# Kernel optimization log

Measured on AMD Instinct MI355X. Metric: run time of the kernel, lower is better.

## Reference

```python
import jax, jax.numpy as jnp
import numpy as np
from functools import partial

N_NODES = 50000
N_EDGES = 1_600_000
T = 9
F_IN = 128
HID = 128
OUT = 1


def setup_inputs() -> dict:
    key = jax.random.key(0)
    ks = jax.random.split(key, 8)
    s = 0.05
    return {
        "x_seq": jax.random.normal(ks[0], (T, N_NODES, F_IN), dtype=jnp.float32),
        "edge_index": jax.random.randint(ks[1], (2, N_EDGES), 0, N_NODES, dtype=jnp.int64),
        "W_gcn": jax.random.normal(ks[2], (F_IN, HID), dtype=jnp.float32) * s,
        "b_gcn": jnp.zeros((HID,), dtype=jnp.float32),
        "W_ih": jax.random.normal(ks[3], (4 * HID, HID), dtype=jnp.float32) * s,
        "W_hh": jax.random.normal(ks[4], (4 * HID, HID), dtype=jnp.float32) * s,
        "b_ih": jnp.zeros((4 * HID,), dtype=jnp.float32),
        "b_hh": jnp.zeros((4 * HID,), dtype=jnp.float32),
        "W_fc": jax.random.normal(ks[5], (HID, OUT), dtype=jnp.float32) * s,
        "b_fc": jnp.zeros((OUT,), dtype=jnp.float32),
    }


def reference(x_seq, edge_index, W_gcn, b_gcn, W_ih, W_hh, b_ih, b_hh, W_fc, b_fc):
    T_, N, _ = x_seq.shape
    H = W_hh.shape[1]

    # --- GCNConv normalization (add self-loops, symmetric deg^-1/2) ---
    loops = jnp.arange(N, dtype=edge_index.dtype)
    src = jnp.concatenate([edge_index[0], loops])  # [E+N]
    dst = jnp.concatenate([edge_index[1], loops])  # [E+N]
    deg = jax.ops.segment_sum(jnp.ones_like(dst, dtype=x_seq.dtype), dst, num_segments=N)
    dinv = jnp.where(deg > 0, jax.lax.rsqrt(deg), 0.0)
    norm = dinv[src] * dinv[dst]  # [E+N]

    # Linear transform for all timesteps at once (dense GEMM)
    xw = jnp.einsum("tnf,fh->tnh", x_seq, W_gcn)  # [T, N, H]

    # Per-timestep gather -> scale -> scatter-add (scan to bound memory)
    def gcn_step(_, xw_t):
        msg = xw_t[src] * norm[:, None]                       # [E+N, H]
        agg = jax.ops.segment_sum(msg, dst, num_segments=N)   # [N, H]
        return None, jax.nn.relu(agg + b_gcn)                 # dropout: eval mode (identity)

    _, emb = jax.lax.scan(gcn_step, None, xw)  # [T, N, H]

    # --- single-layer LSTM over time, nodes as batch (PyTorch gate order i,f,g,o) ---
    def lstm_step(carry, x_t):
        h_prev, c_prev = carry
        gates = x_t @ W_ih.T + h_prev @ W_hh.T + (b_ih + b_hh)  # [N, 4H]
        i, f, g, o = jnp.split(gates, 4, axis=-1)
        i, f, o = jax.nn.sigmoid(i), jax.nn.sigmoid(f), jax.nn.sigmoid(o)
        g = jnp.tanh(g)
        c = f * c_prev + i * g
        h = o * jnp.tanh(c)
        return (h, c), h

    init = (jnp.zeros((N, H), x_seq.dtype), jnp.zeros((N, H), x_seq.dtype))
    _, hs = jax.lax.scan(lstm_step, init, emb)  # [T, N, H]

    lstm_out = jnp.transpose(hs, (1, 0, 2))  # [N, T, H] (batch_first)
    # final_dropout: eval mode (identity)
    return lstm_out @ W_fc + b_fc  # [N, T, OUT]
```

## Files before the change

kernel.cpp:

```cpp
#include <hip/hip_runtime.h>
#include <math.h>

#define NN 50000
#define TT 9
#define FD 128
#define HD 128

using short8 = __attribute__((ext_vector_type(8))) short;
using half8  = __attribute__((ext_vector_type(8))) _Float16;
using f32x4  = __attribute__((ext_vector_type(4))) float;
using f32x2  = __attribute__((ext_vector_type(2))) float;
using half2v = __attribute__((ext_vector_type(2))) _Float16;
typedef unsigned short ushort_t;

__device__ inline float fast_sigmoid(float x) {
  x = fminf(fmaxf(x, -30.f), 30.f);
  return 1.f / (1.f + __expf(-x));
}
__device__ inline float fast_tanh(float x) {
  x = fminf(fmaxf(x, -15.f), 15.f);
  float e = __expf(2.f * x);
  return (e - 1.f) / (e + 1.f);
}

__global__ void k_detect(const unsigned int* __restrict__ e32, int nchk,
                         int* __restrict__ stride_out) {
  __shared__ unsigned int red[256];
  unsigned int acc = 0;
  for (int i = threadIdx.x; i < nchk; i += 256) acc |= e32[2 * i + 1];
  red[threadIdx.x] = acc;
  __syncthreads();
  for (int s = 128; s > 0; s >>= 1) {
    if ((int)threadIdx.x < s) red[threadIdx.x] |= red[threadIdx.x + s];
    __syncthreads();
  }
  if (threadIdx.x == 0) stride_out[0] = (red[0] == 0u) ? 2 : 1;
}

__global__ void k_count(const unsigned int* __restrict__ e32, int E,
                        const int* __restrict__ stridep, int* __restrict__ cnt) {
  int e = blockIdx.x * 256 + threadIdx.x;
  if (e >= E) return;
  int st = stridep[0];
  int d = (int)e32[(size_t)(E + e) * st];
  atomicAdd(&cnt[d], 1);
}

__global__ void k_dinv(const int* __restrict__ cnt, float* __restrict__ dinv, int N) {
  int n = blockIdx.x * 256 + threadIdx.x;
  if (n < N) dinv[n] = rsqrtf((float)(cnt[n] + 1));
}

__global__ void k_scan(const int* __restrict__ cnt, int* __restrict__ rowp, int N) {
  __shared__ int buf[1024];
  __shared__ int carry_s;
  if (threadIdx.x == 0) carry_s = 0;
  __syncthreads();
  for (int base = 0; base < N; base += 1024) {
    int i = base + threadIdx.x;
    int v = (i < N) ? cnt[i] : 0;
    buf[threadIdx.x] = v;
    __syncthreads();
    for (int off = 1; off < 1024; off <<= 1) {
      int t = ((int)threadIdx.x >= off) ? buf[threadIdx.x - off] : 0;
      __syncthreads();
      buf[threadIdx.x] += t;
      __syncthreads();
    }
    int incl = buf[threadIdx.x];
    int carry = carry_s;
    if (i < N) rowp[i] = carry + incl - v;
    __syncthreads();
    if (threadIdx.x == 1023) carry_s = carry + incl;
    __syncthreads();
  }
  if (threadIdx.x == 0) rowp[N] = carry_s;
}

__global__ void k_scatter(const unsigned int* __restrict__ e32, int E,
                          const int* __restrict__ stridep, const int* __restrict__ rowp,
                          int* __restrict__ fill, int* __restrict__ col) {
  int e = blockIdx.x * 256 + threadIdx.x;
  if (e >= E) return;
  int st = stridep[0];
  int s = (int)e32[(size_t)e * st];
  int d = (int)e32[(size_t)(E + e) * st];
  int pos = rowp[d] + atomicAdd(&fill[d], 1);
  col[pos] = s;
}

__global__ __launch_bounds__(256) void k_prep(const float* __restrict__ x,
                                              const float* __restrict__ dinv,
                                              _Float16* __restrict__ xs) {
  int lane = threadIdx.x & 63;
  int n = blockIdx.x * 4 + (threadIdx.x >> 6);
  int t = blockIdx.y;
  float dn = dinv[n];
  f32x2 v = __builtin_nontemporal_load(
      (const f32x2*)(x + ((size_t)t * NN + n) * 128 + lane * 2));
  half2v r;
  r.x = (_Float16)(v.x * dn);
  r.y = (_Float16)(v.y * dn);
  *(half2v*)(xs + ((size_t)t * NN + n) * 128 + lane * 2) = r;
}

__global__ void k_packw(const float* __restrict__ Wih, const float* __restrict__ Whh,
                        const float* __restrict__ bih, const float* __restrict__ bhh,
                        _Float16* __restrict__ Wh_, _Float16* __restrict__ Wl_,
                        float* __restrict__ bsum) {
  int r = blockIdx.x;
  int k = threadIdx.x;
  int ri = (r & 127) * 4 + (r >> 7);
  float v = (k < 128) ? Wih[(size_t)r * 128 + k] : Whh[(size_t)r * 128 + (k - 128)];
  _Float16 hi = (_Float16)v;
  _Float16 lo = (_Float16)(v - (float)hi);
  size_t o = ((size_t)(k >> 3) * 512 + ri) * 8 + (k & 7);
  Wh_[o] = hi;
  Wl_[o] = lo;
  if (k == 0) bsum[ri] = bih[r] + bhh[r];
}

__global__ void k_packg(const float* __restrict__ Wg, _Float16* __restrict__ Gh_,
                        _Float16* __restrict__ Gl_) {
  int h = blockIdx.x, k = threadIdx.x;
  float v = Wg[(size_t)k * 128 + h];
  _Float16 hi = (_Float16)v;
  _Float16 lo = (_Float16)(v - (float)hi);
  size_t o = ((size_t)(k >> 3) * 128 + h) * 8 + (k & 7);
  Gh_[o] = hi;
  Gl_[o] = lo;
}

__global__ __launch_bounds__(256) void k_agg(const _Float16* __restrict__ xs,
                                             const float* __restrict__ dinv,
                                             const int* __restrict__ rowp,
                                             const int* __restrict__ col,
                                             _Float16* __restrict__ agg16) {
  __shared__ unsigned int pk[4][132];
  int lane = threadIdx.x & 63;
  int wv = threadIdx.x >> 6;
  int n = blockIdx.x * 4 + wv;
  int t = blockIdx.y;
  const _Float16* xb = xs + (size_t)t * NN * 128;
  float dn = dinv[n];
  half2v sv = *(const half2v*)(xb + (size_t)n * 128 + lane * 2);
  float ax = (float)sv.x, ay = (float)sv.y;
  int beg = rowp[n], end = rowp[n + 1];
  for (int base = beg; base < end; base += 64) {
    int m = end - base;
    if (m > 64) m = 64;
    int sl = (lane < m) ? col[base + lane] : 0;
    int j = 0;
    for (; j + 8 <= m; j += 8) {
      int s[8];
#pragma unroll
      for (int u = 0; u < 8; ++u) s[u] = __shfl(sl, j + u);
      half2v g[8];
#pragma unroll
      for (int u = 0; u < 8; ++u)
        g[u] = *(const half2v*)(xb + (size_t)s[u] * 128 + lane * 2);
#pragma unroll
      for (int u = 0; u < 8; ++u) {
        ax += (float)g[u].x;
        ay += (float)g[u].y;
      }
    }
    for (; j < m; ++j) {
      int s = __shfl(sl, j);
      half2v g = *(const half2v*)(xb + (size_t)s * 128 + lane * 2);
      ax += (float)g.x;
      ay += (float)g.y;
    }
  }
  half2v r;
  r.x = (_Float16)(ax * dn);
  r.y = (_Float16)(ay * dn);
  union { half2v h; unsigned int u; } cv;
  cv.h = r;
  pk[wv][lane] = cv.u;
  __syncthreads();
  int tid = threadIdx.x;
  if (tid < 64) {
    int g = tid & 3, c = tid >> 2;
    uint4 u4;
    u4.x = pk[g][c * 4 + 0];
    u4.y = pk[g][c * 4 + 1];
    u4.z = pk[g][c * 4 + 2];
    u4.w = pk[g][c * 4 + 3];
    int n2 = blockIdx.x * 4 + g;
    *(uint4*)(agg16 + ((size_t)(c * 9 + t) * NN + n2) * 8) = u4;
  }
}

#define BN 48
#define NCT 3
#define LST 136
__global__ __launch_bounds__(512, 4) void k_fused(
    const _Float16* __restrict__ agg16, const _Float16* __restrict__ Gh_,
    const _Float16* __restrict__ Gl_, const float* __restrict__ bg,
    const _Float16* __restrict__ Wh_, const _Float16* __restrict__ Wl_,
    const float* __restrict__ bsum, const float* __restrict__ Wfc,
    const float* __restrict__ bfc, float* __restrict__ out) {
  __shared__ _Float16 ldsE[BN * LST];
  __shared__ _Float16 ldsH[BN * LST];
  __shared__ float obuf[8][BN];
  int tid = threadIdx.x;
  int w = tid >> 6, lane = tid & 63, q = lane >> 4, cl = lane & 15;
  int n0 = blockIdx.x * BN;
  float cst[4][NCT] = {};
  float bfv = bfc[0];
#pragma unroll 1
  for (int t = 0; t < TT; ++t) {
    {
      f32x4 acce[NCT] = {};
#pragma unroll 2
      for (int ks = 0; ks < 4; ++ks) {
        int chunk = ks * 4 + q;
        size_t wo = ((size_t)chunk * 128 + w * 16 + cl) * 8;
        half8 gah = *(const half8*)(Gh_ + wo);
        half8 gal = *(const half8*)(Gl_ + wo);
#pragma unroll
        for (int ct = 0; ct < NCT; ++ct) {
          int node = n0 + ct * 16 + cl;
          half8 b = {0, 0, 0, 0, 0, 0, 0, 0};
          if (node < NN)
            b = __builtin_nontemporal_load(
                (const half8*)(agg16 + ((size_t)(chunk * 9 + t) * NN + node) * 8));
          acce[ct] = __builtin_amdgcn_mfma_f32_16x16x32_f16(gah, b, acce[ct], 0, 0, 0);
          acce[ct] = __builtin_amdgcn_mfma_f32_16x16x32_f16(gal, b, acce[ct], 0, 0, 0);
        }
      }
#pragma unroll
      for (int ct = 0; ct < NCT; ++ct) {
#pragma unroll
        for (int j = 0; j < 4; ++j) {
          int hid = w * 16 + q * 4 + j;
          float v = acce[ct][j] + bg[hid];
          v = v > 0.f ? v : 0.f;
          ldsE[(ct * 16 + cl) * LST + hid] = (_Float16)v;
        }
      }
    }
    __syncthreads();
    f32x4 acc[4][NCT] = {};
    int ksmax = (t == 0) ? 4 : 8;
#pragma unroll 2
    for (int ks = 0; ks < ksmax; ++ks) {
      int chunk = ks * 4 + q;
      const _Float16* Bp = (ks < 4) ? ldsE : ldsH;
      int kk = (ks & 3) * 32 + q * 8;
      half8 bb[NCT];
#pragma unroll
      for (int ct = 0; ct < NCT; ++ct)
        bb[ct] = *(const half8*)(Bp + (ct * 16 + cl) * LST + kk);
#pragma unroll
      for (int rt = 0; rt < 4; ++rt) {
        size_t ao = ((size_t)chunk * 512 + w * 64 + rt * 16 + cl) * 8;
        half8 ah = *(const half8*)(Wh_ + ao);
        half8 al = *(const half8*)(Wl_ + ao);
#pragma unroll
        for (int ct = 0; ct < NCT; ++ct) {
          acc[rt][ct] = __builtin_amdgcn_mfma_f32_16x16x32_f16(ah, bb[ct], acc[rt][ct], 0, 0, 0);
          acc[rt][ct] = __builtin_amdgcn_mfma_f32_16x16x32_f16(al, bb[ct], acc[rt][ct], 0, 0, 0);
        }
      }
    }
    __syncthreads();
    float op[NCT];
#pragma unroll
    for (int ct = 0; ct < NCT; ++ct) op[ct] = 0.f;
#pragma unroll
    for (int rt = 0; rt < 4; ++rt) {
      int jl = w * 16 + rt * 4 + q;
      float4 bs = *(const float4*)(bsum + jl * 4);
      float wf = Wfc[jl];
#pragma unroll
      for (int ct = 0; ct < NCT; ++ct) {
        float gi = acc[rt][ct][0] + bs.x;
        float gf = acc[rt][ct][1] + bs.y;
        float gg = acc[rt][ct][2] + bs.z;
        float go = acc[rt][ct][3] + bs.w;
        float ig = fast_sigmoid(gi), fg = fast_sigmoid(gf), og = fast_sigmoid(go);
        float gt = fast_tanh(gg);
        float cn = fg * cst[rt][ct] + ig * gt;
        cst[rt][ct] = cn;
        float hn = og * fast_tanh(cn);
        op[ct] += hn * wf;
        ldsH[(ct * 16 + cl) * LST + jl] = (_Float16)hn;
      }
    }
#pragma unroll
    for (int ct = 0; ct < NCT; ++ct) {
      op[ct] += __shfl_xor(op[ct], 16);
      op[ct] += __shfl_xor(op[ct], 32);
    }
    if (q == 0) {
#pragma unroll
      for (int ct = 0; ct < NCT; ++ct) obuf[w][ct * 16 + cl] = op[ct];
    }
    __syncthreads();
    if (tid < BN) {
      int node = n0 + tid;
      if (node < NN) {
        float v = bfv;
#pragma unroll
        for (int ww = 0; ww < 8; ++ww) v += obuf[ww][tid];
        out[(size_t)node * TT + t] = v;
      }
    }
  }
}

static inline size_t alignup(size_t x) { return (x + 511) & ~(size_t)511; }

extern "C" void kernel_launch(void* const* d_in, const int* in_sizes, int n_in,
                              void* d_out, int out_size, void* d_ws, size_t ws_size,
                              hipStream_t stream) {
  const float* x_seq = (const float*)d_in[0];
  const unsigned int* e32 = (const unsigned int*)d_in[1];
  const float* W_gcn = (const float*)d_in[2];
  const float* b_gcn = (const float*)d_in[3];
  const float* W_ih = (const float*)d_in[4];
  const float* W_hh = (const float*)d_in[5];
  const float* b_ih = (const float*)d_in[6];
  const float* b_hh = (const float*)d_in[7];
  const float* W_fc = (const float*)d_in[8];
  const float* b_fc = (const float*)d_in[9];
  float* out = (float*)d_out;

  const int N = NN;
  const int E = in_sizes[1] / 2;

  char* p = (char*)d_ws;
  int* stridep = (int*)p;                    p += 512;
  int* cnt = (int*)p;                        p += alignup((size_t)N * 4);
  int* rowp = (int*)p;                       p += alignup((size_t)(N + 1) * 4);
  int* col = (int*)p;                        p += alignup((size_t)E * 4);
  float* dinv = (float*)p;                   p += alignup((size_t)N * 4);
  _Float16* xs16 = (_Float16*)p;             p += alignup((size_t)9 * N * 128 * 2);
  _Float16* agg16 = (_Float16*)p;            p += alignup((size_t)16 * 9 * N * 8 * 2);
  _Float16* wpkh = (_Float16*)p;             p += alignup((size_t)32 * 512 * 8 * 2);
  _Float16* wpkl = (_Float16*)p;             p += alignup((size_t)32 * 512 * 8 * 2);
  _Float16* wgth = (_Float16*)p;             p += alignup((size_t)16 * 128 * 8 * 2);
  _Float16* wgtl = (_Float16*)p;             p += alignup((size_t)16 * 128 * 8 * 2);
  float* bsum = (float*)p;                   p += alignup((size_t)512 * 4);

  hipMemsetAsync(cnt, 0, (size_t)N * 4, stream);

  int nchk = E < 8192 ? E : 8192;
  k_detect<<<1, 256, 0, stream>>>(e32, nchk, stridep);
  k_count<<<(E + 255) / 256, 256, 0, stream>>>(e32, E, stridep, cnt);
  k_dinv<<<(N + 255) / 256, 256, 0, stream>>>(cnt, dinv, N);
  k_scan<<<1, 1024, 0, stream>>>(cnt, rowp, N);
  hipMemsetAsync(cnt, 0, (size_t)N * 4, stream);
  k_scatter<<<(E + 255) / 256, 256, 0, stream>>>(e32, E, stridep, rowp, cnt, col);
  k_prep<<<dim3(N / 4, 9), 256, 0, stream>>>(x_seq, dinv, xs16);
  k_packw<<<512, 256, 0, stream>>>(W_ih, W_hh, b_ih, b_hh, wpkh, wpkl, bsum);
  k_packg<<<128, 128, 0, stream>>>(W_gcn, wgth, wgtl);

  k_agg<<<dim3(N / 4, 9), 256, 0, stream>>>(xs16, dinv, rowp, col, agg16);
  k_fused<<<(N + BN - 1) / BN, 512, 0, stream>>>(agg16, wgth, wgtl, b_gcn,
                                                 wpkh, wpkl, bsum, W_fc, b_fc, out);
}
```

Measured before the change: 1.661 ms.

## Double-buffer aggregated inputs in LDS via async global_load_lds prefetch

Each timestep's aggregated fp16 input tile is now loaded asynchronously into a double-buffered LDS array with global_load_lds, one step ahead. The MFMA loop then reads from LDS instead of issuing per-wave global loads. Previously all 8 waves redundantly loaded the same node tile, so this cuts duplicate global traffic and hides load latency behind the LSTM compute. It adds 24KB of LDS per block, which may lower occupancy, and it depends on the existing __syncthreads for the async writes to be visible.

```diff
diff --git a/kernel.cpp b/kernel.cpp
--- a/kernel.cpp
+++ b/kernel.cpp
@@ -201,6 +201,7 @@
     const _Float16* __restrict__ Wh_, const _Float16* __restrict__ Wl_,
     const float* __restrict__ bsum, const float* __restrict__ Wfc,
     const float* __restrict__ bfc, float* __restrict__ out) {
+  __shared__ _Float16 ldsA[2][16 * BN * 8];
   __shared__ _Float16 ldsE[BN * LST];
   __shared__ _Float16 ldsH[BN * LST];
   __shared__ float obuf[8][BN];
@@ -209,8 +210,34 @@
   int n0 = blockIdx.x * BN;
   float cst[4][NCT] = {};
   float bfv = bfc[0];
+  int cA = tid / BN, nA = tid - cA * BN;
+  int nodeA = n0 + nA; if (nodeA >= NN) nodeA = NN - 1;
+  int sB = tid + 512;
+  int cB = sB / BN, nB = sB - cB * BN;
+  int nodeB = n0 + nB; if (nodeB >= NN) nodeB = NN - 1;
+
+  __builtin_amdgcn_global_load_lds(
+      (const __attribute__((address_space(1))) void*)(agg16 + ((size_t)(cA * 9 + 0) * NN + nodeA) * 8),
+      (__attribute__((address_space(3))) void*)(&ldsA[0][tid * 8]), 16, 0, 0);
+  if (tid < 256)
+    __builtin_amdgcn_global_load_lds(
+        (const __attribute__((address_space(1))) void*)(agg16 + ((size_t)(cB * 9 + 0) * NN + nodeB) * 8),
+        (__attribute__((address_space(3))) void*)(&ldsA[0][sB * 8]), 16, 0, 0);
+  __syncthreads();
+
 #pragma unroll 1
   for (int t = 0; t < TT; ++t) {
+    const _Float16* Ab = ldsA[t & 1];
+    if (t + 1 < TT) {
+      int bs = (t + 1) & 1;
+      __builtin_amdgcn_global_load_lds(
+          (const __attribute__((address_space(1))) void*)(agg16 + ((size_t)(cA * 9 + (t + 1)) * NN + nodeA) * 8),
+          (__attribute__((address_space(3))) void*)(&ldsA[bs][tid * 8]), 16, 0, 0);
+      if (tid < 256)
+        __builtin_amdgcn_global_load_lds(
+            (const __attribute__((address_space(1))) void*)(agg16 + ((size_t)(cB * 9 + (t + 1)) * NN + nodeB) * 8),
+            (__attribute__((address_space(3))) void*)(&ldsA[bs][sB * 8]), 16, 0, 0);
+    }
     {
       f32x4 acce[NCT] = {};
 #pragma unroll 2
@@ -221,11 +248,7 @@
         half8 gal = *(const half8*)(Gl_ + wo);
 #pragma unroll
         for (int ct = 0; ct < NCT; ++ct) {
-          int node = n0 + ct * 16 + cl;
-          half8 b = {0, 0, 0, 0, 0, 0, 0, 0};
-          if (node < NN)
-            b = __builtin_nontemporal_load(
-                (const half8*)(agg16 + ((size_t)(chunk * 9 + t) * NN + node) * 8));
+          half8 b = *(const half8*)(Ab + (chunk * BN + ct * 16 + cl) * 8);
           acce[ct] = __builtin_amdgcn_mfma_f32_16x16x32_f16(gah, b, acce[ct], 0, 0, 0);
           acce[ct] = __builtin_amdgcn_mfma_f32_16x16x32_f16(gal, b, acce[ct], 0, 0, 0);
         }
```

After: 1.599 ms. -3.7%, faster.
